# Kernel optimization log

Hardware: AMD Instinct MI355X
Metric: run time of the kernel (lower is better)

Reference implementation:

```python
import jax, jax.numpy as jnp
import numpy as np

N_NODES = 50000
N_EDGES = 600000
DIMS = [128, 128, 128]  # input_dim + hidden_dims


def setup_inputs() -> dict:
    key = jax.random.key(0)
    ks = jax.random.split(key, 8)
    node_features = jax.random.normal(ks[0], (N_NODES, DIMS[0]), dtype=jnp.float32)
    edge_index = jax.random.randint(ks[1], (2, N_EDGES), 0, N_NODES, dtype=jnp.int64)
    # GCNConv params: weight [in, out] (glorot-ish), bias [out] (zeros init in PyG; use small randn)
    W1 = jax.random.normal(ks[2], (DIMS[0], DIMS[1]), dtype=jnp.float32) / np.sqrt(DIMS[0])
    b1 = jnp.zeros((DIMS[1],), dtype=jnp.float32)
    W2 = jax.random.normal(ks[3], (DIMS[1], DIMS[2]), dtype=jnp.float32) / np.sqrt(DIMS[1])
    b2 = jnp.zeros((DIMS[2],), dtype=jnp.float32)
    return {"node_features": node_features, "edge_index": edge_index,
            "W1": W1, "b1": b1, "W2": W2, "b2": b2}


def _gcn_norm(edge_index, n_nodes):
    # Add self loops, then symmetric normalization as in PyG gcn_norm.
    loop = jnp.arange(n_nodes, dtype=edge_index.dtype)
    src = jnp.concatenate([edge_index[0], loop])  # message sources (x_j)
    dst = jnp.concatenate([edge_index[1], loop])  # aggregation targets
    deg = jax.ops.segment_sum(jnp.ones_like(dst, dtype=jnp.float32), dst,
                              num_segments=n_nodes)
    dinv = jnp.where(deg > 0, jax.lax.rsqrt(jnp.maximum(deg, 1.0)), 0.0)
    norm = dinv[src] * dinv[dst]  # [E + N]
    return src, dst, norm


def _gcn_layer(x, W, b, src, dst, norm, n_nodes):
    h = x @ W                                  # [N, out]
    msgs = h[src] * norm[:, None]              # gather + scale  [E+N, out]
    out = jax.ops.segment_sum(msgs, dst, num_segments=n_nodes)  # scatter-add
    return out + b


def reference(node_features, edge_index, W1, b1, W2, b2):
    n_nodes = node_features.shape[0]
    src, dst, norm = _gcn_norm(edge_index, n_nodes)
    x = _gcn_layer(node_features, W1, b1, src, dst, norm, n_nodes)
    x = jax.nn.relu(x)  # ReLU between layers, none after last
    x = _gcn_layer(x, W2, b2, src, dst, norm, n_nodes)
    return x
```

## Files before the change

kernel.cpp:

```cpp
#include <hip/hip_runtime.h>
#include <hip/hip_bf16.h>

typedef __bf16 bf16_t;
typedef __bf16 bf16x8 __attribute__((ext_vector_type(8)));
typedef float f32x4 __attribute__((ext_vector_type(4)));
typedef unsigned short u16;

#define DIM 128
#define CAP 64

__global__ void k_scatter_ell(const int* __restrict__ EI, int* __restrict__ cnt,
                              u16* __restrict__ col, int e) {
    __shared__ int any;
    int tid = threadIdx.x;
    long gi = (long)blockIdx.x * 256 + tid;
    if (tid == 0) any = 0;
    __syncthreads();
    bool a = (gi < e);
    int w = a ? EI[2 * gi + 1] : 0;
    if (w) atomicOr(&any, 1);
    __syncthreads();
    bool i64 = (any == 0);
    if (a) {
        int s = i64 ? EI[2 * gi]             : EI[gi];
        int d = i64 ? EI[2 * ((long)e + gi)] : EI[e + gi];
        int pos = atomicAdd(&cnt[d], 1);
        if (pos < CAP) col[(long)d * CAP + pos] = (u16)s;
    }
}

__global__ void k_prep(const float* __restrict__ W1, const float* __restrict__ W2,
                       bf16_t* __restrict__ TH1, bf16_t* __restrict__ TL1,
                       bf16_t* __restrict__ TH2, bf16_t* __restrict__ TL2,
                       const int* __restrict__ cnt, float* __restrict__ dinv, int n) {
    int b = blockIdx.x;
    if (b < 2) {
        const float* W = (b == 0) ? W1 : W2;
        bf16_t* TH = (b == 0) ? TH1 : TH2;
        bf16_t* TL = (b == 0) ? TL1 : TL2;
        for (int idx = threadIdx.x; idx < 128 * 128; idx += 256) {
            int j    = idx & 7;
            int lane = (idx >> 3) & 63;
            int kc   = (idx >> 9) & 3;
            int nt   = idx >> 11;
            int nn = nt * 16 + (lane & 15);
            int k  = kc * 32 + (lane >> 4) * 8 + j;
            float wv = W[k * 128 + nn];
            bf16_t h = (bf16_t)wv;
            TH[idx] = h;
            TL[idx] = (bf16_t)(wv - (float)h);
        }
        return;
    }
    int g = (b - 2) * 256 + threadIdx.x;
    if (g < n) dinv[g] = rsqrtf((float)(cnt[g] + 1));
}

__global__ __launch_bounds__(256) void k_gemm_f32(const float* __restrict__ A,
        const bf16_t* __restrict__ TH, const bf16_t* __restrict__ TL,
        const float* __restrict__ dinv, bf16_t* __restrict__ H, int M) {
    int tid = threadIdx.x;
    int wave = tid >> 6, lane = tid & 63;
    long row_base = ((long)blockIdx.x * 4 + wave) * 16;
    int n16 = lane & 15, quad = lane >> 4;

    bf16x8 a_hi[4], a_lo[4];
    const float* arow = A + (row_base + n16) * DIM + quad * 8;
#pragma unroll
    for (int kc = 0; kc < 4; kc++) {
        float4 p0 = *(const float4*)(arow + kc * 32);
        float4 p1 = *(const float4*)(arow + kc * 32 + 4);
        float v[8] = {p0.x, p0.y, p0.z, p0.w, p1.x, p1.y, p1.z, p1.w};
#pragma unroll
        for (int j = 0; j < 8; j++) {
            bf16_t h = (bf16_t)v[j];
            a_hi[kc][j] = h;
            a_lo[kc][j] = (bf16_t)(v[j] - (float)h);
        }
    }

    float dr[4];
#pragma unroll
    for (int r = 0; r < 4; r++) dr[r] = dinv[row_base + quad * 4 + r];

#pragma unroll
    for (int nt = 0; nt < 8; nt++) {
        f32x4 acc = {0.f, 0.f, 0.f, 0.f};
#pragma unroll
        for (int kc = 0; kc < 4; kc++) {
            long tb = ((long)(nt * 4 + kc) * 64 + lane) * 8;
            bf16x8 bh = *(const bf16x8*)(TH + tb);
            bf16x8 bl = *(const bf16x8*)(TL + tb);
            acc = __builtin_amdgcn_mfma_f32_16x16x32_bf16(a_hi[kc], bh, acc, 0, 0, 0);
            acc = __builtin_amdgcn_mfma_f32_16x16x32_bf16(a_lo[kc], bh, acc, 0, 0, 0);
            acc = __builtin_amdgcn_mfma_f32_16x16x32_bf16(a_hi[kc], bl, acc, 0, 0, 0);
        }
        bf16_t* hrow = H + (row_base + quad * 4) * DIM + nt * 16 + n16;
#pragma unroll
        for (int r = 0; r < 4; r++) hrow[(long)r * DIM] = (bf16_t)(dr[r] * acc[r]);
    }
}

__global__ __launch_bounds__(256) void k_gemm_b16(const bf16_t* __restrict__ A,
        const bf16_t* __restrict__ TH, const bf16_t* __restrict__ TL,
        const float* __restrict__ dinv, bf16_t* __restrict__ H, int M) {
    int tid = threadIdx.x;
    int wave = tid >> 6, lane = tid & 63;
    long row_base = ((long)blockIdx.x * 4 + wave) * 16;
    int n16 = lane & 15, quad = lane >> 4;

    bf16x8 a[4];
    const bf16_t* arow = A + (row_base + n16) * DIM + quad * 8;
#pragma unroll
    for (int kc = 0; kc < 4; kc++) a[kc] = *(const bf16x8*)(arow + kc * 32);

    float dr[4];
#pragma unroll
    for (int r = 0; r < 4; r++) dr[r] = dinv[row_base + quad * 4 + r];

#pragma unroll
    for (int nt = 0; nt < 8; nt++) {
        f32x4 acc = {0.f, 0.f, 0.f, 0.f};
#pragma unroll
        for (int kc = 0; kc < 4; kc++) {
            long tb = ((long)(nt * 4 + kc) * 64 + lane) * 8;
            bf16x8 bh = *(const bf16x8*)(TH + tb);
            bf16x8 bl = *(const bf16x8*)(TL + tb);
            acc = __builtin_amdgcn_mfma_f32_16x16x32_bf16(a[kc], bh, acc, 0, 0, 0);
            acc = __builtin_amdgcn_mfma_f32_16x16x32_bf16(a[kc], bl, acc, 0, 0, 0);
        }
        bf16_t* hrow = H + (row_base + quad * 4) * DIM + nt * 16 + n16;
#pragma unroll
        for (int r = 0; r < 4; r++) hrow[(long)r * DIM] = (bf16_t)(dr[r] * acc[r]);
    }
}

__global__ __launch_bounds__(256) void k_agg(const bf16_t* __restrict__ H,
        const int* __restrict__ cnt, const u16* __restrict__ col,
        const float* __restrict__ dinv, const float* __restrict__ bias,
        float* __restrict__ outf, bf16_t* __restrict__ outb,
        int n, int mode) {
    int lane = threadIdx.x & 63;
    int wave = threadIdx.x >> 6;
    int sub = lane >> 4;
    int sl  = lane & 15;
    int i = (blockIdx.x * 4 + wave) * 4 + sub;
    bool act = (i < n);
    float acc[8] = {0.f, 0.f, 0.f, 0.f, 0.f, 0.f, 0.f, 0.f};
    float d = 0.f;
    int deg = 0;
    const u16* crow = col;
    if (act) {
        d = dinv[i];
        deg = cnt[i];
        if (deg > CAP) deg = CAP;
        crow = col + (long)i * CAP;
        bf16x8 hs = *(const bf16x8*)(H + (long)i * DIM + sl * 8);
#pragma unroll
        for (int q = 0; q < 8; q++) acc[q] = (float)hs[q];
    }
    int j = 0;
    for (; j + 4 <= deg; j += 4) {
        ushort4 ss = *(const ushort4*)(crow + j);
        bf16x8 h0 = *(const bf16x8*)(H + (long)ss.x * DIM + sl * 8);
        bf16x8 h1 = *(const bf16x8*)(H + (long)ss.y * DIM + sl * 8);
        bf16x8 h2 = *(const bf16x8*)(H + (long)ss.z * DIM + sl * 8);
        bf16x8 h3 = *(const bf16x8*)(H + (long)ss.w * DIM + sl * 8);
#pragma unroll
        for (int q = 0; q < 8; q++)
            acc[q] += ((float)h0[q] + (float)h1[q]) + ((float)h2[q] + (float)h3[q]);
    }
    for (; j < deg; j++) {
        int s0 = crow[j];
        bf16x8 h0 = *(const bf16x8*)(H + (long)s0 * DIM + sl * 8);
#pragma unroll
        for (int q = 0; q < 8; q++) acc[q] += (float)h0[q];
    }
    if (act) {
        float4 b0 = *(const float4*)(bias + sl * 8);
        float4 b1 = *(const float4*)(bias + sl * 8 + 4);
        float r[8];
        r[0] = d * acc[0] + b0.x; r[1] = d * acc[1] + b0.y;
        r[2] = d * acc[2] + b0.z; r[3] = d * acc[3] + b0.w;
        r[4] = d * acc[4] + b1.x; r[5] = d * acc[5] + b1.y;
        r[6] = d * acc[6] + b1.z; r[7] = d * acc[7] + b1.w;
        if (mode == 1) {
#pragma unroll
            for (int q = 0; q < 8; q++) r[q] = fmaxf(r[q], 0.f);
            bf16x8 o;
#pragma unroll
            for (int q = 0; q < 8; q++) o[q] = (bf16_t)r[q];
            *(bf16x8*)(outb + (long)i * DIM + sl * 8) = o;
        } else {
            float* op = outf + (long)i * DIM + sl * 8;
            *(float4*)op       = make_float4(r[0], r[1], r[2], r[3]);
            *(float4*)(op + 4) = make_float4(r[4], r[5], r[6], r[7]);
        }
    }
}

extern "C" void kernel_launch(void* const* d_in, const int* in_sizes, int n_in,
                              void* d_out, int out_size, void* d_ws, size_t ws_size,
                              hipStream_t stream) {
    const float* X  = (const float*)d_in[0];
    const int*   EI = (const int*)d_in[1];
    const float* W1 = (const float*)d_in[2];
    const float* B1 = (const float*)d_in[3];
    const float* W2 = (const float*)d_in[4];
    const float* B2 = (const float*)d_in[5];
    float* OUT = (float*)d_out;

    const int N = in_sizes[0] / DIM;
    const int E = in_sizes[1] / 2;
    (void)n_in; (void)out_size; (void)ws_size;

    char* w = (char*)d_ws;
    auto alloc = [&](size_t bytes) -> char* {
        char* p = w;
        w += (bytes + 255) & ~(size_t)255;
        return p;
    };
    int*    cnt  = (int*)alloc((size_t)N * 4);
    float*  dinv = (float*)alloc((size_t)N * 4);
    u16*    col  = (u16*)alloc((size_t)N * CAP * 2);
    bf16_t* TH1  = (bf16_t*)alloc(128 * 128 * 2);
    bf16_t* TL1  = (bf16_t*)alloc(128 * 128 * 2);
    bf16_t* TH2  = (bf16_t*)alloc(128 * 128 * 2);
    bf16_t* TL2  = (bf16_t*)alloc(128 * 128 * 2);
    bf16_t* H    = (bf16_t*)alloc((size_t)N * DIM * 2);
    bf16_t* X1b  = (bf16_t*)alloc((size_t)N * DIM * 2);

    int gE = (E + 255) / 256;
    int gN = (N + 255) / 256;
    int GB = (N + 63) / 64;
    int gA = (N + 15) / 16;

    hipMemsetAsync(cnt, 0, (size_t)N * 4, stream);
    k_scatter_ell<<<gE, 256, 0, stream>>>(EI, cnt, col, E);
    k_prep<<<gN + 2, 256, 0, stream>>>(W1, W2, TH1, TL1, TH2, TL2, cnt, dinv, N);
    k_gemm_f32<<<GB, 256, 0, stream>>>(X, TH1, TL1, dinv, H, N);
    k_agg<<<gA, 256, 0, stream>>>(H, cnt, col, dinv, B1, nullptr, X1b, N, 1);
    k_gemm_b16<<<GB, 256, 0, stream>>>(X1b, TH2, TL2, dinv, H, N);
    k_agg<<<gA, 256, 0, stream>>>(H, cnt, col, dinv, B2, OUT, nullptr, N, 0);
}
```

Baseline: 210.7 us.

## Fuse edge scatter with first GEMM and defer source degree scaling to aggregation

The edge-list ELL scatter now runs in the same launch as the first-layer GEMM, split by block index, so the atomic-heavy graph build overlaps the X·W1 MFMA work. Because dinv is no longer available during that GEMM, the source-side normalisation moves into the first aggregation as a per-neighbour dinv gather and multiply. dinv is computed in its own small kernel, and the weight prep becomes a separate 2-block launch. This trades one fewer serial dependency for extra per-edge dinv loads and an added kernel launch.

```diff
diff --git a/kernel.cpp b/kernel.cpp
--- a/kernel.cpp
+++ b/kernel.cpp
@@ -9,59 +9,54 @@
 #define DIM 128
 #define CAP 64
 
-__global__ void k_scatter_ell(const int* __restrict__ EI, int* __restrict__ cnt,
-                              u16* __restrict__ col, int e) {
-    __shared__ int any;
-    int tid = threadIdx.x;
-    long gi = (long)blockIdx.x * 256 + tid;
-    if (tid == 0) any = 0;
-    __syncthreads();
-    bool a = (gi < e);
-    int w = a ? EI[2 * gi + 1] : 0;
-    if (w) atomicOr(&any, 1);
-    __syncthreads();
-    bool i64 = (any == 0);
-    if (a) {
-        int s = i64 ? EI[2 * gi]             : EI[gi];
-        int d = i64 ? EI[2 * ((long)e + gi)] : EI[e + gi];
-        int pos = atomicAdd(&cnt[d], 1);
-        if (pos < CAP) col[(long)d * CAP + pos] = (u16)s;
-    }
-}
-
 __global__ void k_prep(const float* __restrict__ W1, const float* __restrict__ W2,
                        bf16_t* __restrict__ TH1, bf16_t* __restrict__ TL1,
-                       bf16_t* __restrict__ TH2, bf16_t* __restrict__ TL2,
-                       const int* __restrict__ cnt, float* __restrict__ dinv, int n) {
+                       bf16_t* __restrict__ TH2, bf16_t* __restrict__ TL2) {
     int b = blockIdx.x;
-    if (b < 2) {
-        const float* W = (b == 0) ? W1 : W2;
-        bf16_t* TH = (b == 0) ? TH1 : TH2;
-        bf16_t* TL = (b == 0) ? TL1 : TL2;
-        for (int idx = threadIdx.x; idx < 128 * 128; idx += 256) {
-            int j    = idx & 7;
-            int lane = (idx >> 3) & 63;
-            int kc   = (idx >> 9) & 3;
-            int nt   = idx >> 11;
-            int nn = nt * 16 + (lane & 15);
-            int k  = kc * 32 + (lane >> 4) * 8 + j;
-            float wv = W[k * 128 + nn];
-            bf16_t h = (bf16_t)wv;
-            TH[idx] = h;
-            TL[idx] = (bf16_t)(wv - (float)h);
+    const float* W = (b == 0) ? W1 : W2;
+    bf16_t* TH = (b == 0) ? TH1 : TH2;
+    bf16_t* TL = (b == 0) ? TL1 : TL2;
+    for (int idx = threadIdx.x; idx < 128 * 128; idx += 256) {
+        int j    = idx & 7;
+        int lane = (idx >> 3) & 63;
+        int kc   = (idx >> 9) & 3;
+        int nt   = idx >> 11;
+        int nn = nt * 16 + (lane & 15);
+        int k  = kc * 32 + (lane >> 4) * 8 + j;
+        float wv = W[k * 128 + nn];
+        bf16_t h = (bf16_t)wv;
+        TH[idx] = h;
+        TL[idx] = (bf16_t)(wv - (float)h);
+    }
+}
+
+__global__ __launch_bounds__(256) void k_front(
+        const bf16_t* __restrict__ TH1, const bf16_t* __restrict__ TL1,
+        const float* __restrict__ A, bf16_t* __restrict__ H, int M, int GB,
+        const int* __restrict__ EI, int* __restrict__ cnt, u16* __restrict__ col, int e) {
+    int b = blockIdx.x;
+    int tid = threadIdx.x;
+    if (b >= GB) {
+        __shared__ int any;
+        long gi = (long)(b - GB) * 256 + tid;
+        if (tid == 0) any = 0;
+        __syncthreads();
+        bool a = (gi < e);
+        int w = a ? EI[2 * gi + 1] : 0;
+        if (w) atomicOr(&any, 1);
+        __syncthreads();
+        bool i64 = (any == 0);
+        if (a) {
+            int s = i64 ? EI[2 * gi]             : EI[gi];
+            int d = i64 ? EI[2 * ((long)e + gi)] : EI[e + gi];
+            int pos = atomicAdd(&cnt[d], 1);
+            if (pos < CAP) col[(long)d * CAP + pos] = (u16)s;
         }
         return;
     }
-    int g = (b - 2) * 256 + threadIdx.x;
-    if (g < n) dinv[g] = rsqrtf((float)(cnt[g] + 1));
-}
-
-__global__ __launch_bounds__(256) void k_gemm_f32(const float* __restrict__ A,
-        const bf16_t* __restrict__ TH, const bf16_t* __restrict__ TL,
-        const float* __restrict__ dinv, bf16_t* __restrict__ H, int M) {
-    int tid = threadIdx.x;
     int wave = tid >> 6, lane = tid & 63;
-    long row_base = ((long)blockIdx.x * 4 + wave) * 16;
+    long row_base = ((long)b * 4 + wave) * 16;
+    if (row_base >= M) return;
     int n16 = lane & 15, quad = lane >> 4;
 
     bf16x8 a_hi[4], a_lo[4];
@@ -78,68 +73,33 @@
             a_lo[kc][j] = (bf16_t)(v[j] - (float)h);
         }
     }
-
-    float dr[4];
-#pragma unroll
-    for (int r = 0; r < 4; r++) dr[r] = dinv[row_base + quad * 4 + r];
-
 #pragma unroll
     for (int nt = 0; nt < 8; nt++) {
         f32x4 acc = {0.f, 0.f, 0.f, 0.f};
 #pragma unroll
         for (int kc = 0; kc < 4; kc++) {
             long tb = ((long)(nt * 4 + kc) * 64 + lane) * 8;
-            bf16x8 bh = *(const bf16x8*)(TH + tb);
-            bf16x8 bl = *(const bf16x8*)(TL + tb);
+            bf16x8 bh = *(const bf16x8*)(TH1 + tb);
+            bf16x8 bl = *(const bf16x8*)(TL1 + tb);
             acc = __builtin_amdgcn_mfma_f32_16x16x32_bf16(a_hi[kc], bh, acc, 0, 0, 0);
             acc = __builtin_amdgcn_mfma_f32_16x16x32_bf16(a_lo[kc], bh, acc, 0, 0, 0);
             acc = __builtin_amdgcn_mfma_f32_16x16x32_bf16(a_hi[kc], bl, acc, 0, 0, 0);
         }
         bf16_t* hrow = H + (row_base + quad * 4) * DIM + nt * 16 + n16;
 #pragma unroll
-        for (int r = 0; r < 4; r++) hrow[(long)r * DIM] = (bf16_t)(dr[r] * acc[r]);
-    }
-}
-
-__global__ __launch_bounds__(256) void k_gemm_b16(const bf16_t* __restrict__ A,
-        const bf16_t* __restrict__ TH, const bf16_t* __restrict__ TL,
-        const float* __restrict__ dinv, bf16_t* __restrict__ H, int M) {
-    int tid = threadIdx.x;
-    int wave = tid >> 6, lane = tid & 63;
-    long row_base = ((long)blockIdx.x * 4 + wave) * 16;
-    int n16 = lane & 15, quad = lane >> 4;
-
-    bf16x8 a[4];
-    const bf16_t* arow = A + (row_base + n16) * DIM + quad * 8;
-#pragma unroll
-    for (int kc = 0; kc < 4; kc++) a[kc] = *(const bf16x8*)(arow + kc * 32);
-
-    float dr[4];
-#pragma unroll
-    for (int r = 0; r < 4; r++) dr[r] = dinv[row_base + quad * 4 + r];
-
-#pragma unroll
-    for (int nt = 0; nt < 8; nt++) {
-        f32x4 acc = {0.f, 0.f, 0.f, 0.f};
-#pragma unroll
-        for (int kc = 0; kc < 4; kc++) {
-            long tb = ((long)(nt * 4 + kc) * 64 + lane) * 8;
-            bf16x8 bh = *(const bf16x8*)(TH + tb);
-            bf16x8 bl = *(const bf16x8*)(TL + tb);
-            acc = __builtin_amdgcn_mfma_f32_16x16x32_bf16(a[kc], bh, acc, 0, 0, 0);
-            acc = __builtin_amdgcn_mfma_f32_16x16x32_bf16(a[kc], bl, acc, 0, 0, 0);
-        }
-        bf16_t* hrow = H + (row_base + quad * 4) * DIM + nt * 16 + n16;
-#pragma unroll
-        for (int r = 0; r < 4; r++) hrow[(long)r * DIM] = (bf16_t)(dr[r] * acc[r]);
-    }
-}
-
-__global__ __launch_bounds__(256) void k_agg(const bf16_t* __restrict__ H,
+        for (int r = 0; r < 4; r++) hrow[(long)r * DIM] = (bf16_t)acc[r];
+    }
+}
+
+__global__ void k_dinv(const int* __restrict__ cnt, float* __restrict__ dinv, int n) {
+    int g = blockIdx.x * 256 + threadIdx.x;
+    if (g < n) dinv[g] = rsqrtf((float)(cnt[g] + 1));
+}
+
+__global__ __launch_bounds__(256) void k_agg1(const bf16_t* __restrict__ H,
         const int* __restrict__ cnt, const u16* __restrict__ col,
         const float* __restrict__ dinv, const float* __restrict__ bias,
-        float* __restrict__ outf, bf16_t* __restrict__ outb,
-        int n, int mode) {
+        bf16_t* __restrict__ outb, int n) {
     int lane = threadIdx.x & 63;
     int wave = threadIdx.x >> 6;
     int sub = lane >> 4;
@@ -157,6 +117,99 @@
         crow = col + (long)i * CAP;
         bf16x8 hs = *(const bf16x8*)(H + (long)i * DIM + sl * 8);
 #pragma unroll
+        for (int q = 0; q < 8; q++) acc[q] = d * (float)hs[q];
+    }
+    int j = 0;
+    for (; j + 4 <= deg; j += 4) {
+        ushort4 ss = *(const ushort4*)(crow + j);
+        float w0 = dinv[ss.x], w1 = dinv[ss.y], w2 = dinv[ss.z], w3 = dinv[ss.w];
+        bf16x8 h0 = *(const bf16x8*)(H + (long)ss.x * DIM + sl * 8);
+        bf16x8 h1 = *(const bf16x8*)(H + (long)ss.y * DIM + sl * 8);
+        bf16x8 h2 = *(const bf16x8*)(H + (long)ss.z * DIM + sl * 8);
+        bf16x8 h3 = *(const bf16x8*)(H + (long)ss.w * DIM + sl * 8);
+#pragma unroll
+        for (int q = 0; q < 8; q++)
+            acc[q] += (w0 * (float)h0[q] + w1 * (float)h1[q])
+                    + (w2 * (float)h2[q] + w3 * (float)h3[q]);
+    }
+    for (; j < deg; j++) {
+        int s0 = crow[j];
+        float w0 = dinv[s0];
+        bf16x8 h0 = *(const bf16x8*)(H + (long)s0 * DIM + sl * 8);
+#pragma unroll
+        for (int q = 0; q < 8; q++) acc[q] += w0 * (float)h0[q];
+    }
+    if (act) {
+        float4 b0 = *(const float4*)(bias + sl * 8);
+        float4 b1 = *(const float4*)(bias + sl * 8 + 4);
+        float r[8];
+        r[0] = d * acc[0] + b0.x; r[1] = d * acc[1] + b0.y;
+        r[2] = d * acc[2] + b0.z; r[3] = d * acc[3] + b0.w;
+        r[4] = d * acc[4] + b1.x; r[5] = d * acc[5] + b1.y;
+        r[6] = d * acc[6] + b1.z; r[7] = d * acc[7] + b1.w;
+        bf16x8 o;
+#pragma unroll
+        for (int q = 0; q < 8; q++) o[q] = (bf16_t)fmaxf(r[q], 0.f);
+        *(bf16x8*)(outb + (long)i * DIM + sl * 8) = o;
+    }
+}
+
+__global__ __launch_bounds__(256) void k_gemm_b16(const bf16_t* __restrict__ A,
+        const bf16_t* __restrict__ TH, const bf16_t* __restrict__ TL,
+        const float* __restrict__ dinv, bf16_t* __restrict__ H, int M) {
+    int tid = threadIdx.x;
+    int wave = tid >> 6, lane = tid & 63;
+    long row_base = ((long)blockIdx.x * 4 + wave) * 16;
+    if (row_base >= M) return;
+    int n16 = lane & 15, quad = lane >> 4;
+
+    bf16x8 a[4];
+    const bf16_t* arow = A + (row_base + n16) * DIM + quad * 8;
+#pragma unroll
+    for (int kc = 0; kc < 4; kc++) a[kc] = *(const bf16x8*)(arow + kc * 32);
+
+    float dr[4];
+#pragma unroll
+    for (int r = 0; r < 4; r++) dr[r] = dinv[row_base + quad * 4 + r];
+
+#pragma unroll
+    for (int nt = 0; nt < 8; nt++) {
+        f32x4 acc = {0.f, 0.f, 0.f, 0.f};
+#pragma unroll
+        for (int kc = 0; kc < 4; kc++) {
+            long tb = ((long)(nt * 4 + kc) * 64 + lane) * 8;
+            bf16x8 bh = *(const bf16x8*)(TH + tb);
+            bf16x8 bl = *(const bf16x8*)(TL + tb);
+            acc = __builtin_amdgcn_mfma_f32_16x16x32_bf16(a[kc], bh, acc, 0, 0, 0);
+            acc = __builtin_amdgcn_mfma_f32_16x16x32_bf16(a[kc], bl, acc, 0, 0, 0);
+        }
+        bf16_t* hrow = H + (row_base + quad * 4) * DIM + nt * 16 + n16;
+#pragma unroll
+        for (int r = 0; r < 4; r++) hrow[(long)r * DIM] = (bf16_t)(dr[r] * acc[r]);
+    }
+}
+
+__global__ __launch_bounds__(256) void k_agg2(const bf16_t* __restrict__ H,
+        const int* __restrict__ cnt, const u16* __restrict__ col,
+        const float* __restrict__ dinv, const float* __restrict__ bias,
+        float* __restrict__ outf, int n) {
+    int lane = threadIdx.x & 63;
+    int wave = threadIdx.x >> 6;
+    int sub = lane >> 4;
+    int sl  = lane & 15;
+    int i = (blockIdx.x * 4 + wave) * 4 + sub;
+    bool act = (i < n);
+    float acc[8] = {0.f, 0.f, 0.f, 0.f, 0.f, 0.f, 0.f, 0.f};
+    float d = 0.f;
+    int deg = 0;
+    const u16* crow = col;
+    if (act) {
+        d = dinv[i];
+        deg = cnt[i];
+        if (deg > CAP) deg = CAP;
+        crow = col + (long)i * CAP;
+        bf16x8 hs = *(const bf16x8*)(H + (long)i * DIM + sl * 8);
+#pragma unroll
         for (int q = 0; q < 8; q++) acc[q] = (float)hs[q];
     }
     int j = 0;
@@ -179,23 +232,11 @@
     if (act) {
         float4 b0 = *(const float4*)(bias + sl * 8);
         float4 b1 = *(const float4*)(bias + sl * 8 + 4);
-        float r[8];
-        r[0] = d * acc[0] + b0.x; r[1] = d * acc[1] + b0.y;
-        r[2] = d * acc[2] + b0.z; r[3] = d * acc[3] + b0.w;
-        r[4] = d * acc[4] + b1.x; r[5] = d * acc[5] + b1.y;
-        r[6] = d * acc[6] + b1.z; r[7] = d * acc[7] + b1.w;
-        if (mode == 1) {
-#pragma unroll
-            for (int q = 0; q < 8; q++) r[q] = fmaxf(r[q], 0.f);
-            bf16x8 o;
-#pragma unroll
-            for (int q = 0; q < 8; q++) o[q] = (bf16_t)r[q];
-            *(bf16x8*)(outb + (long)i * DIM + sl * 8) = o;
-        } else {
-            float* op = outf + (long)i * DIM + sl * 8;
-            *(float4*)op       = make_float4(r[0], r[1], r[2], r[3]);
-            *(float4*)(op + 4) = make_float4(r[4], r[5], r[6], r[7]);
-        }
+        float* op = outf + (long)i * DIM + sl * 8;
+        *(float4*)op = make_float4(d * acc[0] + b0.x, d * acc[1] + b0.y,
+                                   d * acc[2] + b0.z, d * acc[3] + b0.w);
+        *(float4*)(op + 4) = make_float4(d * acc[4] + b1.x, d * acc[5] + b1.y,
+                                         d * acc[6] + b1.z, d * acc[7] + b1.w);
     }
 }
 
@@ -227,7 +268,8 @@
     bf16_t* TL1  = (bf16_t*)alloc(128 * 128 * 2);
     bf16_t* TH2  = (bf16_t*)alloc(128 * 128 * 2);
     bf16_t* TL2  = (bf16_t*)alloc(128 * 128 * 2);
-    bf16_t* H    = (bf16_t*)alloc((size_t)N * DIM * 2);
+    bf16_t* H1   = (bf16_t*)alloc((size_t)N * DIM * 2);
+    bf16_t* H2   = (bf16_t*)alloc((size_t)N * DIM * 2);
     bf16_t* X1b  = (bf16_t*)alloc((size_t)N * DIM * 2);
 
     int gE = (E + 255) / 256;
@@ -236,10 +278,10 @@
     int gA = (N + 15) / 16;
 
     hipMemsetAsync(cnt, 0, (size_t)N * 4, stream);
-    k_scatter_ell<<<gE, 256, 0, stream>>>(EI, cnt, col, E);
-    k_prep<<<gN + 2, 256, 0, stream>>>(W1, W2, TH1, TL1, TH2, TL2, cnt, dinv, N);
-    k_gemm_f32<<<GB, 256, 0, stream>>>(X, TH1, TL1, dinv, H, N);
-    k_agg<<<gA, 256, 0, stream>>>(H, cnt, col, dinv, B1, nullptr, X1b, N, 1);
-    k_gemm_b16<<<GB, 256, 0, stream>>>(X1b, TH2, TL2, dinv, H, N);
-    k_agg<<<gA, 256, 0, stream>>>(H, cnt, col, dinv, B2, OUT, nullptr, N, 0);
-}
+    k_prep<<<2, 256, 0, stream>>>(W1, W2, TH1, TL1, TH2, TL2);
+    k_front<<<GB + gE, 256, 0, stream>>>(TH1, TL1, X, H1, N, GB, EI, cnt, col, E);
+    k_dinv<<<gN, 256, 0, stream>>>(cnt, dinv, N);
+    k_agg1<<<gA, 256, 0, stream>>>(H1, cnt, col, dinv, B1, X1b, N);
+    k_gemm_b16<<<GB, 256, 0, stream>>>(X1b, TH2, TL2, dinv, H2, N);
+    k_agg2<<<gA, 256, 0, stream>>>(H2, cnt, col, dinv, B2, OUT, N);
+}
```

New measurement: 200.9 us. -4.6%, faster.
